# Kernel tuning notes

Measured on AMD Instinct MI355X. Metric: run time of the kernel, lower is better.

Reference implementation:

```python
import jax, jax.numpy as jnp
import numpy as np

WS = 8  # window size (module uses window_sizes as a scalar)


def setup_inputs() -> dict:
    key = jax.random.key(0)
    ks = jax.random.split(key, 4)
    b, c, h, w = 4, 128, 256, 256
    x = jax.random.normal(ks[0], (b, c, h, w), jnp.float32)
    w_qkv = jax.random.normal(ks[1], (3 * c, c), jnp.float32) * (1.0 / np.sqrt(c))
    w_dw = jax.random.normal(ks[2], (3 * c, 1, 3, 3), jnp.float32) * (1.0 / 3.0)
    w_proj = jax.random.normal(ks[3], (c, c), jnp.float32) * (1.0 / np.sqrt(c))
    temperature = jnp.ones((1, 1, 1), jnp.float32)
    return {"x": x, "w_qkv": w_qkv, "w_dw": w_dw, "w_proj": w_proj,
            "temperature": temperature}


def _window(t, ws):
    # b c (h dh) (w dw) -> b (h w) (dh dw) c
    b, c, H, W = t.shape
    t = t.reshape(b, c, H // ws, ws, W // ws, ws)
    return t.transpose(0, 2, 4, 3, 5, 1).reshape(b, (H // ws) * (W // ws), ws * ws, c)


def _unwindow(t, ws, H, W):
    # b (h w) (dh dw) c -> b c (h dh) (w dw)
    b = t.shape[0]
    c = t.shape[-1]
    t = t.reshape(b, H // ws, W // ws, ws, ws, c)
    return t.transpose(0, 5, 1, 3, 2, 4).reshape(b, c, H, W)


def reference(x, w_qkv, w_dw, w_proj, temperature):
    b, c, H, W = x.shape
    ws = WS
    sh = -ws // 2  # = -(ws//2) for even ws, matching torch.roll shifts
    x_ = jnp.roll(x, (sh, sh), axis=(2, 3))
    # 1x1 conv c -> 3c
    qkv = jnp.einsum('oc,bchw->bohw', w_qkv, x_)
    # depthwise 3x3, padding 1
    qkv = jax.lax.conv_general_dilated(
        qkv, w_dw, window_strides=(1, 1), padding=[(1, 1), (1, 1)],
        dimension_numbers=('NCHW', 'OIHW', 'NCHW'), feature_group_count=3 * c)
    q, k, v = jnp.split(qkv, 3, axis=1)
    q = _window(q, ws)  # [b, nW, ws*ws, c]
    k = _window(k, ws)
    v = _window(v, ws)
    # L2-normalize along channel dim (torch F.normalize, eps=1e-12)
    q = q / jnp.maximum(jnp.linalg.norm(q, axis=-1, keepdims=True), 1e-12)
    k = k / jnp.maximum(jnp.linalg.norm(k, axis=-1, keepdims=True), 1e-12)
    # channel-wise attention: [b, nW, c, c]
    attn = jnp.einsum('bnpc,bnpd->bncd', q, k) * temperature.reshape(())
    attn = jax.nn.relu(attn)
    out = jnp.einsum('bnpc,bncd->bnpd', v, attn)  # [b, nW, ws*ws, c]
    out = _unwindow(out, ws, H, W)
    out = jnp.roll(out, (ws // 2, ws // 2), axis=(2, 3))
    y = jnp.einsum('oc,bchw->bohw', w_proj, out)
    return (y, attn)
```

## Files before the change

### kernel.cpp

```cpp
#include <hip/hip_runtime.h>
#include <hip/hip_bf16.h>

constexpr int NB = 4;
constexpr int CC = 128;
constexpr int HW = 65536;

using bf16x8 = __attribute__((ext_vector_type(8))) short;
using f32x4  = __attribute__((ext_vector_type(4))) float;

__device__ __forceinline__ unsigned short f2bf(float f) {
  unsigned u = __builtin_bit_cast(unsigned, f);
  u += 0x7FFFu + ((u >> 16) & 1u);
  return (unsigned short)(u >> 16);
}
__device__ __forceinline__ float bf2f(unsigned short s) {
  return __builtin_bit_cast(float, (unsigned)s << 16);
}

__device__ __forceinline__ void stage_halo_vec(const __hip_bfloat16* __restrict__ base,
                                               int ih0, int iw0, int t,
                                               unsigned short* __restrict__ halo) {
#pragma unroll
  for (int it = 0; it < 15; ++it) {
    int idx = it * 256 + t;
    int ch = idx / 30;
    int rem = idx - ch * 30;
    int r = rem / 3;
    int c = rem - r * 3;
    int ii = ih0 - 1 + r;
    int j0 = iw0 - 8 + c * 8;
    uint4 v = {0u, 0u, 0u, 0u};
    if ((unsigned)ii < 256u && (unsigned)j0 <= 248u)
      v = *(const uint4*)(base + (((size_t)ch) << 16) + (ii << 8) + j0);
    unsigned short* hrow = halo + ch * 168 + r * 16;
    if (c == 1) {
      *(uint4*)hrow = v;
    } else if (c == 0) {
      hrow[9] = (unsigned short)(v.w >> 16);
    } else {
      hrow[8] = (unsigned short)(v.x & 0xFFFFu);
    }
  }
}

__device__ __forceinline__ void dw_row(const unsigned short* __restrict__ halo,
                                       const float* __restrict__ wd,
                                       int ch, int pr, float* __restrict__ outv) {
#pragma unroll
  for (int pc = 0; pc < 8; ++pc) outv[pc] = 0.f;
#pragma unroll
  for (int kr = 0; kr < 3; ++kr) {
    const unsigned short* hrow = halo + ch * 168 + (pr + kr) * 16;
    uint4 rw = *(const uint4*)hrow;
    float rv[10];
    rv[0] = bf2f((unsigned short)(rw.x & 0xFFFFu));
    rv[1] = bf2f((unsigned short)(rw.x >> 16));
    rv[2] = bf2f((unsigned short)(rw.y & 0xFFFFu));
    rv[3] = bf2f((unsigned short)(rw.y >> 16));
    rv[4] = bf2f((unsigned short)(rw.z & 0xFFFFu));
    rv[5] = bf2f((unsigned short)(rw.z >> 16));
    rv[6] = bf2f((unsigned short)(rw.w & 0xFFFFu));
    rv[7] = bf2f((unsigned short)(rw.w >> 16));
    rv[8] = bf2f(hrow[8]);
    rv[9] = bf2f(hrow[9]);
#pragma unroll
    for (int s = 0; s < 3; ++s) {
      float wv = wd[kr * 3 + s];
#pragma unroll
      for (int pc = 0; pc < 8; ++pc) {
        int m = pc + s - 1;
        float xv = (m < 0) ? rv[9] : rv[m];
        outv[pc] = fmaf(wv, xv, outv[pc]);
      }
    }
  }
}

__global__ __launch_bounds__(256) void k_qkv_mfma(const float* __restrict__ x,
                                                  const float* __restrict__ wq,
                                                  __hip_bfloat16* __restrict__ qkv) {
  __shared__ unsigned short x_s[128 * 136];

  int blk = blockIdx.x;
  int b = blk >> 9, i = (blk >> 1) & 255, jh = blk & 1;
  int j0 = jh << 7;
  int si = (i + 4) & 255;
  int t = threadIdx.x;

  {
    int c0 = (t & 63) << 1;
    int jb = (t >> 6) << 5;
    const float* xr0 = x + (((size_t)(b * CC + c0)) << 16) + (si << 8);
    const float* xr1 = xr0 + HW;
#pragma unroll
    for (int u = 0; u < 8; ++u) {
      int jj = jb + (u << 2);
      int sj = j0 + jj + 4;
      float v0[4], v1[4];
      if (sj + 3 <= 255) {
        *(float4*)v0 = *(const float4*)(xr0 + sj);
        *(float4*)v1 = *(const float4*)(xr1 + sj);
      } else {
#pragma unroll
        for (int e = 0; e < 4; ++e) {
          int s = (sj + e) & 255;
          v0[e] = xr0[s];
          v1[e] = xr1[s];
        }
      }
#pragma unroll
      for (int e = 0; e < 4; ++e) {
        unsigned pk = (unsigned)f2bf(v0[e]) | ((unsigned)f2bf(v1[e]) << 16);
        *(unsigned*)&x_s[(jj + e) * 136 + c0] = pk;
      }
    }
  }
  __syncthreads();

  int w = t >> 6;
  int lane = t & 63;
  int col = lane & 15;
  int kg = lane >> 4;

#pragma unroll 1
  for (int oi = 0; oi < 3; ++oi) {
    int m0 = oi * 128 + w * 32;
    bf16x8 afr[2][4];
#pragma unroll
    for (int mt = 0; mt < 2; ++mt) {
      const float* wr = wq + (m0 + mt * 16 + col) * CC + kg * 8;
#pragma unroll
      for (int ks = 0; ks < 4; ++ks) {
        float wa[4], wb[4];
        *(float4*)wa = *(const float4*)(wr + ks * 32);
        *(float4*)wb = *(const float4*)(wr + ks * 32 + 4);
        bf16x8 f;
#pragma unroll
        for (int e = 0; e < 4; ++e) {
          f[e] = (short)f2bf(wa[e]);
          f[e + 4] = (short)f2bf(wb[e]);
        }
        afr[mt][ks] = f;
      }
    }
#pragma unroll 1
    for (int n = 0; n < 8; ++n) {
      int px = n * 16 + col;
      f32x4 acc0 = {0.f, 0.f, 0.f, 0.f};
      f32x4 acc1 = {0.f, 0.f, 0.f, 0.f};
#pragma unroll
      for (int ks = 0; ks < 4; ++ks) {
        bf16x8 bfr = *(const bf16x8*)&x_s[px * 136 + ks * 32 + kg * 8];
        acc0 = __builtin_amdgcn_mfma_f32_16x16x32_bf16(afr[0][ks], bfr, acc0, 0, 0, 0);
        acc1 = __builtin_amdgcn_mfma_f32_16x16x32_bf16(afr[1][ks], bfr, acc1, 0, 0, 0);
      }
      int j = j0 + n * 16 + col;
#pragma unroll
      for (int r = 0; r < 4; ++r) {
        int och0 = m0 + kg * 4 + r;
        int och1 = m0 + 16 + kg * 4 + r;
        int g0 = och0 >> 7, c0 = och0 & 127;
        int g1 = och1 >> 7, c1 = och1 & 127;
        qkv[(((size_t)((g0 * NB + b) * CC + c0)) << 16) + (i << 8) + j] =
            __float2bfloat16(acc0[r]);
        qkv[(((size_t)((g1 * NB + b) * CC + c1)) << 16) + (i << 8) + j] =
            __float2bfloat16(acc1[r]);
      }
    }
  }
}

__global__ __launch_bounds__(256) void k_attn(const __hip_bfloat16* __restrict__ qkv,
                                              const float* __restrict__ wdw,
                                              const float* __restrict__ temp_p,
                                              float* __restrict__ attn_out) {
  __shared__ unsigned short halo_s[128 * 168];
  __shared__ unsigned short q_t[128][72];
  __shared__ unsigned short k_t[128][72];
  __shared__ float sumsq_s[64];
  __shared__ float ps[64];

  int blk = blockIdx.x;
  int b = blk >> 10, n = blk & 1023;
  int ih0 = (n >> 5) << 3, iw0 = (n & 31) << 3;
  int t = threadIdx.x;
  int ch_l = t & 15, grp = t >> 4;
  float tau = temp_p[0];

#pragma unroll 1
  for (int g = 0; g < 2; ++g) {
    __syncthreads();
    if (t < 64) sumsq_s[t] = 0.f;
    stage_halo_vec(qkv + (((size_t)((g * NB + b) * CC)) << 16), ih0, iw0, t, halo_s);
    __syncthreads();

    float outv[4][8];
#pragma unroll
    for (int it = 0; it < 4; ++it) {
      int task = grp + it * 16;
      int ch = ((task >> 3) << 4) + ch_l;
      int pr = task & 7;
      float wd[9];
#pragma unroll
      for (int kk = 0; kk < 9; ++kk) wd[kk] = wdw[(g * CC + ch) * 9 + kk];
      dw_row(halo_s, wd, ch, pr, outv[it]);
#pragma unroll
      for (int pc = 0; pc < 8; ++pc) {
        float sq = outv[it][pc] * outv[it][pc];
        sq += __shfl_xor(sq, 1);
        sq += __shfl_xor(sq, 2);
        sq += __shfl_xor(sq, 4);
        sq += __shfl_xor(sq, 8);
        if (ch_l == 0) atomicAdd(&sumsq_s[pr * 8 + pc], sq);
      }
    }
    __syncthreads();
    if (t < 64) {
      float nr = fmaxf(sqrtf(sumsq_s[t]), 1e-12f);
      ps[t] = g ? (tau / nr) : (1.f / nr);
    }
    __syncthreads();
    unsigned short (*dst)[72] = g ? k_t : q_t;
#pragma unroll
    for (int it = 0; it < 4; ++it) {
      int task = grp + it * 16;
      int ch = ((task >> 3) << 4) + ch_l;
      int pr = task & 7;
      unsigned short o8[8];
#pragma unroll
      for (int pc = 0; pc < 8; ++pc)
        o8[pc] = f2bf(outv[it][pc] * ps[pr * 8 + pc]);
      *(uint4*)&dst[ch][pr * 8] = *(const uint4*)o8;
    }
  }
  __syncthreads();

  int wv = t >> 6, lane = t & 63;
  int col = lane & 15, kg = lane >> 4;
  int c0 = wv * 32;
  bf16x8 afr[2][2];
#pragma unroll
  for (int mt = 0; mt < 2; ++mt)
#pragma unroll
    for (int ks = 0; ks < 2; ++ks)
      afr[mt][ks] = *(const bf16x8*)&q_t[c0 + mt * 16 + col][ks * 32 + kg * 8];
  float* ao = attn_out + ((size_t)blk << 14);
#pragma unroll
  for (int dt = 0; dt < 8; ++dt) {
    bf16x8 b0 = *(const bf16x8*)&k_t[dt * 16 + col][kg * 8];
    bf16x8 b1 = *(const bf16x8*)&k_t[dt * 16 + col][32 + kg * 8];
    f32x4 a0 = {0.f, 0.f, 0.f, 0.f};
    f32x4 a1 = {0.f, 0.f, 0.f, 0.f};
    a0 = __builtin_amdgcn_mfma_f32_16x16x32_bf16(afr[0][0], b0, a0, 0, 0, 0);
    a0 = __builtin_amdgcn_mfma_f32_16x16x32_bf16(afr[0][1], b1, a0, 0, 0, 0);
    a1 = __builtin_amdgcn_mfma_f32_16x16x32_bf16(afr[1][0], b0, a1, 0, 0, 0);
    a1 = __builtin_amdgcn_mfma_f32_16x16x32_bf16(afr[1][1], b1, a1, 0, 0, 0);
#pragma unroll
    for (int r = 0; r < 4; ++r) {
      ao[((c0 + kg * 4 + r) << 7) + dt * 16 + col] = fmaxf(a0[r], 0.f);
      ao[((c0 + 16 + kg * 4 + r) << 7) + dt * 16 + col] = fmaxf(a1[r], 0.f);
    }
  }
}

__global__ __launch_bounds__(256) void k_pv(const __hip_bfloat16* __restrict__ qkv,
                                            const float* __restrict__ wdw,
                                            const float* __restrict__ attn,
                                            __hip_bfloat16* __restrict__ out_win) {
  __shared__ unsigned short halo_s[128 * 168];
  __shared__ unsigned short v_t[64][136];
  __shared__ unsigned short a_t[128][40];

  int blk = blockIdx.x;
  int b = blk >> 10, n = blk & 1023;
  int ih0 = (n >> 5) << 3, iw0 = (n & 31) << 3;
  int t = threadIdx.x;
  int ch_l = t & 15, grp = t >> 4;

  stage_halo_vec(qkv + (((size_t)((2 * NB + b) * CC)) << 16), ih0, iw0, t, halo_s);
  __syncthreads();
#pragma unroll
  for (int it = 0; it < 4; ++it) {
    int task = grp + it * 16;
    int ch = ((task >> 3) << 4) + ch_l;
    int pr = task & 7;
    float wd[9];
#pragma unroll
    for (int kk = 0; kk < 9; ++kk) wd[kk] = wdw[(2 * CC + ch) * 9 + kk];
    float outv[8];
    dw_row(halo_s, wd, ch, pr, outv);
#pragma unroll
    for (int pc = 0; pc < 8; ++pc)
      v_t[pr * 8 + pc][ch] = f2bf(outv[pc]);
  }

  int wv = t >> 6, lane = t & 63;
  int col = lane & 15, kg = lane >> 4;
  f32x4 acc[8];
#pragma unroll
  for (int dt = 0; dt < 8; ++dt) acc[dt] = {0.f, 0.f, 0.f, 0.f};
  const float* ab = attn + ((size_t)blk << 14);
#pragma unroll 1
  for (int ks = 0; ks < 4; ++ks) {
    __syncthreads();
#pragma unroll
    for (int it = 0; it < 2; ++it) {
      int idx = it * 256 + t;
      int d4 = idx & 31, cp = idx >> 5;
      const float* ar = ab + (((size_t)(ks * 32 + cp * 2)) << 7) + d4 * 4;
      float4 r0 = *(const float4*)ar;
      float4 r1 = *(const float4*)(ar + 128);
      float a0a[4] = {r0.x, r0.y, r0.z, r0.w};
      float a1a[4] = {r1.x, r1.y, r1.z, r1.w};
#pragma unroll
      for (int e = 0; e < 4; ++e) {
        unsigned pk = (unsigned)f2bf(a0a[e]) | ((unsigned)f2bf(a1a[e]) << 16);
        *(unsigned*)&a_t[d4 * 4 + e][cp * 2] = pk;
      }
    }
    __syncthreads();
    bf16x8 va = *(const bf16x8*)&v_t[wv * 16 + col][ks * 32 + kg * 8];
#pragma unroll
    for (int dt = 0; dt < 8; ++dt) {
      bf16x8 bf = *(const bf16x8*)&a_t[dt * 16 + col][kg * 8];
      acc[dt] = __builtin_amdgcn_mfma_f32_16x16x32_bf16(va, bf, acc[dt], 0, 0, 0);
    }
  }
  __hip_bfloat16* ow = out_win + ((size_t)blk << 13);
#pragma unroll
  for (int dt = 0; dt < 8; ++dt)
#pragma unroll
    for (int r = 0; r < 4; ++r)
      ow[((wv * 16 + kg * 4 + r) << 7) + dt * 16 + col] = __float2bfloat16(acc[dt][r]);
}

__global__ __launch_bounds__(256) void k_proj_mfma(const __hip_bfloat16* __restrict__ out_win,
                                                   const float* __restrict__ wp,
                                                   float* __restrict__ y) {
  __shared__ unsigned short w_s[128 * 136];

  int t = threadIdx.x;
  {
    int och = t >> 1, ch0 = (t & 1) << 6;
    const float* wr = wp + och * CC + ch0;
#pragma unroll
    for (int u = 0; u < 32; ++u) {
      float2 v = *(const float2*)(wr + 2 * u);
      unsigned pk = (unsigned)f2bf(v.x) | ((unsigned)f2bf(v.y) << 16);
      *(unsigned*)&w_s[och * 136 + ch0 + 2 * u] = pk;
    }
  }
  __syncthreads();

  int w = t >> 6, lane = t & 63;
  int col = lane & 15, kg = lane >> 4;
  int bn = blockIdx.x * 4 + w;
  int b = bn >> 10, n = bn & 1023;
  const __hip_bfloat16* ob = out_win + ((size_t)bn << 13);

  bf16x8 afr[8][4];
#pragma unroll
  for (int mt = 0; mt < 8; ++mt)
#pragma unroll
    for (int ks = 0; ks < 4; ++ks)
      afr[mt][ks] = *(const bf16x8*)&w_s[(mt * 16 + col) * 136 + ks * 32 + kg * 8];

#pragma unroll 1
  for (int nt = 0; nt < 4; ++nt) {
    int p = nt * 16 + col;
    bf16x8 bfr[4];
#pragma unroll
    for (int ks = 0; ks < 4; ++ks)
      bfr[ks] = *(const bf16x8*)(ob + p * CC + ks * 32 + kg * 8);
    int i_f = (((n >> 5) << 3) + (p >> 3) + 4) & 255;
    int j_f = (((n & 31) << 3) + (p & 7) + 4) & 255;
    float* yp = y + (((size_t)b * CC) << 16) + (i_f << 8) + j_f;
#pragma unroll
    for (int mt = 0; mt < 8; ++mt) {
      f32x4 acc = {0.f, 0.f, 0.f, 0.f};
#pragma unroll
      for (int ks = 0; ks < 4; ++ks)
        acc = __builtin_amdgcn_mfma_f32_16x16x32_bf16(afr[mt][ks], bfr[ks], acc, 0, 0, 0);
#pragma unroll
      for (int r = 0; r < 4; ++r) {
        int och = mt * 16 + kg * 4 + r;
        yp[(size_t)och << 16] = acc[r];
      }
    }
  }
}

extern "C" void kernel_launch(void* const* d_in, const int* in_sizes, int n_in,
                              void* d_out, int out_size, void* d_ws, size_t ws_size,
                              hipStream_t stream) {
  const float* x = (const float*)d_in[0];
  const float* w_qkv = (const float*)d_in[1];
  const float* w_dw = (const float*)d_in[2];
  const float* w_proj = (const float*)d_in[3];
  const float* temp = (const float*)d_in[4];
  float* y = (float*)d_out;
  float* attn = (float*)d_out + (size_t)NB * CC * HW;

  __hip_bfloat16* qkv = (__hip_bfloat16*)d_ws;
  __hip_bfloat16* out_win = (__hip_bfloat16*)d_ws;

  k_qkv_mfma<<<2048, 256, 0, stream>>>(x, w_qkv, qkv);
  k_attn<<<4096, 256, 0, stream>>>(qkv, w_dw, temp, attn);
  k_pv<<<4096, 256, 0, stream>>>(qkv, w_dw, attn, out_win);
  k_proj_mfma<<<1024, 256, 0, stream>>>(out_win, w_proj, y);
}
```

Before: 753.6 us.

## Prefetch K halo and attn tiles into registers, swizzle a_t in reused halo LDS

In k_attn the Q and K passes are unrolled. The K halo is loaded into registers while the Q depthwise conv runs, and the atomicAdd-based sum of squares becomes a per-thread fma accumulation with one shuffle reduction and a two-slot shared sum. In k_pv the whole attn tile is prefetched into registers before the V depthwise conv, then written once into the reused halo LDS with an XOR swizzle, which removes the per-k-step barriers. This hides global latency and cuts syncs and LDS bank conflicts, at the cost of much higher register pressure (15 uint4 plus 16 float4 held per thread), which may lower occupancy.

Measured after the change: 676.8 us. 10.2% less time.

```diff
diff --git a/kernel.cpp b/kernel.cpp
--- a/kernel.cpp
+++ b/kernel.cpp
@@ -17,30 +17,30 @@
   return __builtin_bit_cast(float, (unsigned)s << 16);
 }
 
-__device__ __forceinline__ void stage_halo_vec(const __hip_bfloat16* __restrict__ base,
-                                               int ih0, int iw0, int t,
-                                               unsigned short* __restrict__ halo) {
-#pragma unroll
-  for (int it = 0; it < 15; ++it) {
-    int idx = it * 256 + t;
-    int ch = idx / 30;
-    int rem = idx - ch * 30;
-    int r = rem / 3;
-    int c = rem - r * 3;
-    int ii = ih0 - 1 + r;
-    int j0 = iw0 - 8 + c * 8;
-    uint4 v = {0u, 0u, 0u, 0u};
-    if ((unsigned)ii < 256u && (unsigned)j0 <= 248u)
-      v = *(const uint4*)(base + (((size_t)ch) << 16) + (ii << 8) + j0);
-    unsigned short* hrow = halo + ch * 168 + r * 16;
-    if (c == 1) {
-      *(uint4*)hrow = v;
-    } else if (c == 0) {
-      hrow[9] = (unsigned short)(v.w >> 16);
-    } else {
-      hrow[8] = (unsigned short)(v.x & 0xFFFFu);
-    }
-  }
+__device__ __forceinline__ void halo_decomp(int idx, int& ch, int& r, int& c) {
+  ch = idx / 30;
+  int rem = idx - ch * 30;
+  r = rem / 3;
+  c = rem - r * 3;
+}
+__device__ __forceinline__ uint4 halo_load_one(const __hip_bfloat16* __restrict__ base,
+                                               int ih0, int iw0, int idx) {
+  int ch, r, c;
+  halo_decomp(idx, ch, r, c);
+  int ii = ih0 - 1 + r, j0 = iw0 - 8 + c * 8;
+  uint4 v = {0u, 0u, 0u, 0u};
+  if ((unsigned)ii < 256u && (unsigned)j0 <= 248u)
+    v = *(const uint4*)(base + (((size_t)ch) << 16) + (ii << 8) + j0);
+  return v;
+}
+__device__ __forceinline__ void halo_store_one(unsigned short* __restrict__ halo,
+                                               int idx, uint4 v) {
+  int ch, r, c;
+  halo_decomp(idx, ch, r, c);
+  unsigned short* hrow = halo + ch * 168 + r * 16;
+  if (c == 1) *(uint4*)hrow = v;
+  else if (c == 0) hrow[9] = (unsigned short)(v.w >> 16);
+  else hrow[8] = (unsigned short)(v.x & 0xFFFFu);
 }
 
 __device__ __forceinline__ void dw_row(const unsigned short* __restrict__ halo,
@@ -177,60 +177,121 @@
   __shared__ unsigned short halo_s[128 * 168];
   __shared__ unsigned short q_t[128][72];
   __shared__ unsigned short k_t[128][72];
-  __shared__ float sumsq_s[64];
-  __shared__ float ps[64];
+  __shared__ float sumsq_s[2][64];
 
   int blk = blockIdx.x;
   int b = blk >> 10, n = blk & 1023;
   int ih0 = (n >> 5) << 3, iw0 = (n & 31) << 3;
   int t = threadIdx.x;
   int ch_l = t & 15, grp = t >> 4;
+  int pr = grp & 7, contrib = grp >> 3;
   float tau = temp_p[0];
-
-#pragma unroll 1
-  for (int g = 0; g < 2; ++g) {
-    __syncthreads();
-    if (t < 64) sumsq_s[t] = 0.f;
-    stage_halo_vec(qkv + (((size_t)((g * NB + b) * CC)) << 16), ih0, iw0, t, halo_s);
-    __syncthreads();
-
-    float outv[4][8];
+  const __hip_bfloat16* qbase = qkv + (((size_t)(b * CC)) << 16);
+  const __hip_bfloat16* kbase = qkv + (((size_t)((NB + b) * CC)) << 16);
+
+#pragma unroll
+  for (int it = 0; it < 15; ++it) {
+    int idx = it * 256 + t;
+    halo_store_one(halo_s, idx, halo_load_one(qbase, ih0, iw0, idx));
+  }
+  __syncthreads();
+
+  uint4 kpre[15];
+#pragma unroll
+  for (int it = 0; it < 15; ++it)
+    kpre[it] = halo_load_one(kbase, ih0, iw0, it * 256 + t);
+
+  float outv[4][8];
+  float ssq[8];
+#pragma unroll
+  for (int pc = 0; pc < 8; ++pc) ssq[pc] = 0.f;
+#pragma unroll
+  for (int it = 0; it < 4; ++it) {
+    int ch = ((contrib + 2 * it) << 4) + ch_l;
+    float wd[9];
+#pragma unroll
+    for (int kk = 0; kk < 9; ++kk) wd[kk] = wdw[ch * 9 + kk];
+    dw_row(halo_s, wd, ch, pr, outv[it]);
+#pragma unroll
+    for (int pc = 0; pc < 8; ++pc) ssq[pc] = fmaf(outv[it][pc], outv[it][pc], ssq[pc]);
+  }
+#pragma unroll
+  for (int pc = 0; pc < 8; ++pc) {
+    float s = ssq[pc];
+    s += __shfl_xor(s, 1);
+    s += __shfl_xor(s, 2);
+    s += __shfl_xor(s, 4);
+    s += __shfl_xor(s, 8);
+    ssq[pc] = s;
+  }
+  if (ch_l == 0) {
+#pragma unroll
+    for (int pc = 0; pc < 8; ++pc) sumsq_s[contrib][pr * 8 + pc] = ssq[pc];
+  }
+  __syncthreads();
+
+#pragma unroll
+  for (int it = 0; it < 15; ++it) halo_store_one(halo_s, it * 256 + t, kpre[it]);
+
+  {
+    float psv[8];
+#pragma unroll
+    for (int pc = 0; pc < 8; ++pc) {
+      float s = sumsq_s[0][pr * 8 + pc] + sumsq_s[1][pr * 8 + pc];
+      psv[pc] = 1.f / fmaxf(sqrtf(s), 1e-12f);
+    }
 #pragma unroll
     for (int it = 0; it < 4; ++it) {
-      int task = grp + it * 16;
-      int ch = ((task >> 3) << 4) + ch_l;
-      int pr = task & 7;
-      float wd[9];
-#pragma unroll
-      for (int kk = 0; kk < 9; ++kk) wd[kk] = wdw[(g * CC + ch) * 9 + kk];
-      dw_row(halo_s, wd, ch, pr, outv[it]);
-#pragma unroll
-      for (int pc = 0; pc < 8; ++pc) {
-        float sq = outv[it][pc] * outv[it][pc];
-        sq += __shfl_xor(sq, 1);
-        sq += __shfl_xor(sq, 2);
-        sq += __shfl_xor(sq, 4);
-        sq += __shfl_xor(sq, 8);
-        if (ch_l == 0) atomicAdd(&sumsq_s[pr * 8 + pc], sq);
-      }
-    }
-    __syncthreads();
-    if (t < 64) {
-      float nr = fmaxf(sqrtf(sumsq_s[t]), 1e-12f);
-      ps[t] = g ? (tau / nr) : (1.f / nr);
-    }
-    __syncthreads();
-    unsigned short (*dst)[72] = g ? k_t : q_t;
+      int ch = ((contrib + 2 * it) << 4) + ch_l;
+      unsigned short o8[8];
+#pragma unroll
+      for (int pc = 0; pc < 8; ++pc) o8[pc] = f2bf(outv[it][pc] * psv[pc]);
+      *(uint4*)&q_t[ch][pr * 8] = *(const uint4*)o8;
+    }
+  }
+  __syncthreads();
+
+#pragma unroll
+  for (int pc = 0; pc < 8; ++pc) ssq[pc] = 0.f;
+#pragma unroll
+  for (int it = 0; it < 4; ++it) {
+    int ch = ((contrib + 2 * it) << 4) + ch_l;
+    float wd[9];
+#pragma unroll
+    for (int kk = 0; kk < 9; ++kk) wd[kk] = wdw[(CC + ch) * 9 + kk];
+    dw_row(halo_s, wd, ch, pr, outv[it]);
+#pragma unroll
+    for (int pc = 0; pc < 8; ++pc) ssq[pc] = fmaf(outv[it][pc], outv[it][pc], ssq[pc]);
+  }
+#pragma unroll
+  for (int pc = 0; pc < 8; ++pc) {
+    float s = ssq[pc];
+    s += __shfl_xor(s, 1);
+    s += __shfl_xor(s, 2);
+    s += __shfl_xor(s, 4);
+    s += __shfl_xor(s, 8);
+    ssq[pc] = s;
+  }
+  if (ch_l == 0) {
+#pragma unroll
+    for (int pc = 0; pc < 8; ++pc) sumsq_s[contrib][pr * 8 + pc] = ssq[pc];
+  }
+  __syncthreads();
+
+  {
+    float psv[8];
+#pragma unroll
+    for (int pc = 0; pc < 8; ++pc) {
+      float s = sumsq_s[0][pr * 8 + pc] + sumsq_s[1][pr * 8 + pc];
+      psv[pc] = tau / fmaxf(sqrtf(s), 1e-12f);
+    }
 #pragma unroll
     for (int it = 0; it < 4; ++it) {
-      int task = grp + it * 16;
-      int ch = ((task >> 3) << 4) + ch_l;
-      int pr = task & 7;
+      int ch = ((contrib + 2 * it) << 4) + ch_l;
       unsigned short o8[8];
 #pragma unroll
-      for (int pc = 0; pc < 8; ++pc)
-        o8[pc] = f2bf(outv[it][pc] * ps[pr * 8 + pc]);
-      *(uint4*)&dst[ch][pr * 8] = *(const uint4*)o8;
+      for (int pc = 0; pc < 8; ++pc) o8[pc] = f2bf(outv[it][pc] * psv[pc]);
+      *(uint4*)&k_t[ch][pr * 8] = *(const uint4*)o8;
     }
   }
   __syncthreads();
@@ -263,66 +324,85 @@
   }
 }
 
+__device__ __forceinline__ int at_addr(int d, int cbyte) {
+  int a = d * 272 + cbyte;
+  return a ^ (((d >> 2) & 7) << 4);
+}
+
 __global__ __launch_bounds__(256) void k_pv(const __hip_bfloat16* __restrict__ qkv,
                                             const float* __restrict__ wdw,
                                             const float* __restrict__ attn,
                                             __hip_bfloat16* __restrict__ out_win) {
   __shared__ unsigned short halo_s[128 * 168];
   __shared__ unsigned short v_t[64][136];
-  __shared__ unsigned short a_t[128][40];
 
   int blk = blockIdx.x;
   int b = blk >> 10, n = blk & 1023;
   int ih0 = (n >> 5) << 3, iw0 = (n & 31) << 3;
   int t = threadIdx.x;
   int ch_l = t & 15, grp = t >> 4;
-
-  stage_halo_vec(qkv + (((size_t)((2 * NB + b) * CC)) << 16), ih0, iw0, t, halo_s);
-  __syncthreads();
+  int pr = grp & 7, contrib = grp >> 3;
+  const __hip_bfloat16* vbase = qkv + (((size_t)((2 * NB + b) * CC)) << 16);
+
+#pragma unroll
+  for (int it = 0; it < 15; ++it) {
+    int idx = it * 256 + t;
+    halo_store_one(halo_s, idx, halo_load_one(vbase, ih0, iw0, idx));
+  }
+  __syncthreads();
+
+  const float* ab = attn + ((size_t)blk << 14);
+  float4 apre[8][2];
+#pragma unroll
+  for (int it = 0; it < 8; ++it) {
+    int idx = it * 256 + t;
+    int d4 = idx & 31, cp = idx >> 5;
+    const float* ar = ab + ((2 * cp) << 7) + 4 * d4;
+    apre[it][0] = *(const float4*)ar;
+    apre[it][1] = *(const float4*)(ar + 128);
+  }
+
 #pragma unroll
   for (int it = 0; it < 4; ++it) {
-    int task = grp + it * 16;
-    int ch = ((task >> 3) << 4) + ch_l;
-    int pr = task & 7;
+    int ch = ((contrib + 2 * it) << 4) + ch_l;
     float wd[9];
 #pragma unroll
     for (int kk = 0; kk < 9; ++kk) wd[kk] = wdw[(2 * CC + ch) * 9 + kk];
     float outv[8];
     dw_row(halo_s, wd, ch, pr, outv);
 #pragma unroll
-    for (int pc = 0; pc < 8; ++pc)
-      v_t[pr * 8 + pc][ch] = f2bf(outv[pc]);
-  }
+    for (int pc = 0; pc < 8; ++pc) v_t[pr * 8 + pc][ch] = f2bf(outv[pc]);
+  }
+  __syncthreads();
+
+  unsigned short* a_t = halo_s;
+#pragma unroll
+  for (int it = 0; it < 8; ++it) {
+    int idx = it * 256 + t;
+    int d4 = idx & 31, cp = idx >> 5;
+    float lo[4], hi[4];
+    *(float4*)lo = apre[it][0];
+    *(float4*)hi = apre[it][1];
+#pragma unroll
+    for (int e = 0; e < 4; ++e) {
+      unsigned pk = (unsigned)f2bf(lo[e]) | ((unsigned)f2bf(hi[e]) << 16);
+      *(unsigned*)((char*)a_t + at_addr(4 * d4 + e, 4 * cp)) = pk;
+    }
+  }
+  __syncthreads();
 
   int wv = t >> 6, lane = t & 63;
   int col = lane & 15, kg = lane >> 4;
   f32x4 acc[8];
 #pragma unroll
   for (int dt = 0; dt < 8; ++dt) acc[dt] = {0.f, 0.f, 0.f, 0.f};
-  const float* ab = attn + ((size_t)blk << 14);
-#pragma unroll 1
+#pragma unroll
   for (int ks = 0; ks < 4; ++ks) {
-    __syncthreads();
-#pragma unroll
-    for (int it = 0; it < 2; ++it) {
-      int idx = it * 256 + t;
-      int d4 = idx & 31, cp = idx >> 5;
-      const float* ar = ab + (((size_t)(ks * 32 + cp * 2)) << 7) + d4 * 4;
-      float4 r0 = *(const float4*)ar;
-      float4 r1 = *(const float4*)(ar + 128);
-      float a0a[4] = {r0.x, r0.y, r0.z, r0.w};
-      float a1a[4] = {r1.x, r1.y, r1.z, r1.w};
-#pragma unroll
-      for (int e = 0; e < 4; ++e) {
-        unsigned pk = (unsigned)f2bf(a0a[e]) | ((unsigned)f2bf(a1a[e]) << 16);
-        *(unsigned*)&a_t[d4 * 4 + e][cp * 2] = pk;
-      }
-    }
-    __syncthreads();
     bf16x8 va = *(const bf16x8*)&v_t[wv * 16 + col][ks * 32 + kg * 8];
 #pragma unroll
     for (int dt = 0; dt < 8; ++dt) {
-      bf16x8 bf = *(const bf16x8*)&a_t[dt * 16 + col][kg * 8];
+      bf16x8 bf = *(const bf16x8*)((const char*)a_t +
+                                   at_addr(dt * 16 + col, (ks * 32 + kg * 8) * 2));
       acc[dt] = __builtin_amdgcn_mfma_f32_16x16x32_bf16(va, bf, acc[dt], 0, 0, 0);
     }
   }
```
